# Kernel tuning notes

Hardware: AMD Instinct MI355X
Metric: run time of the kernel (lower is better)

Reference implementation:

```python
import jax, jax.numpy as jnp
import numpy as np

ALPHA = 0.9
T = 809          # doc_len_limit hard-coded in fofe_tricontext_encoder
M = 16           # opt['max_len'] (cand_len_limit)
BN_EPS = 1e-5


def _cand_indices(T, M):
    # Enumeration order matches get_sample_index: outer over start s, inner over span.
    s_list, e_list = [], []
    for s in range(T):
        for span in range(min(M, T - s)):
            s_list.append(s)
            e_list.append(s + span)
    return np.asarray(s_list, np.int32), np.asarray(e_list, np.int32)

_S_IDX, _E_IDX = _cand_indices(T, M)          # [N_CANDS] = [12824]
_SPAN = (_E_IDX - _S_IDX).astype(np.int64)
# FOFE decay coefficient alpha^(e-s+1) for subtracting the prefix before the span
_COEF = (ALPHA ** (_SPAN + 1)).astype(np.float32)
# Lower-triangular FOFE prefix operator: A[t,k] = alpha^(t-k) for k<=t
_DIFF = np.subtract.outer(np.arange(T), np.arange(T))
_AFWD = np.where(_DIFF >= 0, ALPHA ** np.maximum(_DIFF, 0), 0.0).astype(np.float32)


def _bn(x, g, b, m, v):
    return (x - m) * jax.lax.rsqrt(v + BN_EPS) * g + b


def _forward(doc_emb, query_emb, W1, g1, b1, m1, v1, W2, g2, b2, m2, v2, W3):
    B, Tt, Dd = doc_emb.shape
    A = jnp.asarray(_AFWD)
    # forward FOFE prefixes F[t] = sum_{k<=t} alpha^(t-k) x[k]; inverse FOFE suffixes
    F = jnp.einsum('tk,bkd->btd', A, doc_emb)          # [B,T,Dd]
    R = jnp.einsum('tk,bkd->btd', A.T, doc_emb)        # [B,T,Dd]
    Fp = jnp.concatenate([jnp.zeros((B, 1, Dd), F.dtype), F], axis=1)   # Fp[:,s]=F[s-1]
    Rp = jnp.concatenate([R, jnp.zeros((B, 1, Dd), R.dtype)], axis=1)   # Rp[:,e+1]
    s_idx = jnp.asarray(_S_IDX)
    e_idx = jnp.asarray(_E_IDX)
    coef = jnp.asarray(_COEF)
    lctx = Fp[:, s_idx]                                 # left context excl cand
    cand = F[:, e_idx] - coef[None, :, None] * Fp[:, s_idx]  # FOFE of span [s,e]
    rctx = Rp[:, e_idx + 1]                             # right context excl cand
    doc_fofe = jnp.concatenate([lctx, cand, rctx], axis=-1)  # [B,N,3*Dd]
    # query FOFE (fofe_linear): z = sum_t alpha^(Lq-1-t) q[t]
    Lq = query_emb.shape[1]
    w = (ALPHA ** jnp.arange(Lq - 1, -1, -1, dtype=jnp.float32))
    qf = jnp.einsum('t,btd->bd', w, query_emb)          # [B,E]
    N = doc_fofe.shape[1]
    qf_b = jnp.broadcast_to(qf[:, None, :], (B, N, qf.shape[-1]))
    dq = jnp.concatenate([doc_fofe, qf_b], axis=-1)     # [B,N,3*Dd+E]
    x = dq.reshape(B * N, -1)
    h = jax.nn.relu(_bn(x @ W1.T, g1, b1, m1, v1))      # 1x1 conv == GEMM
    h = jax.nn.relu(_bn(h @ W2.T, g2, b2, m2, v2))
    out = (h @ W3.T).reshape(B, N, 2)                   # 2 class scores per candidate
    return out


def setup_inputs() -> dict:
    key = jax.random.key(0)
    ks = jax.random.split(key, 13)
    B, Lq, Dd, E = 4, 30, 304, 300
    Cin, H4, H2 = 3 * Dd + E, 1024, 512
    return {
        'doc_emb': jax.random.normal(ks[0], (B, T, Dd), jnp.float32),
        'query_emb': jax.random.normal(ks[1], (B, Lq, E), jnp.float32),
        'W1': jax.random.normal(ks[2], (H4, Cin), jnp.float32) / np.sqrt(Cin),
        'g1': jax.random.normal(ks[3], (H4,), jnp.float32),
        'b1': jax.random.normal(ks[4], (H4,), jnp.float32),
        'm1': jax.random.normal(ks[5], (H4,), jnp.float32),
        'v1': jax.random.uniform(ks[6], (H4,), jnp.float32),
        'W2': jax.random.normal(ks[7], (H2, H4), jnp.float32) / np.sqrt(H4),
        'g2': jax.random.normal(ks[8], (H2,), jnp.float32),
        'b2': jax.random.normal(ks[9], (H2,), jnp.float32),
        'm2': jax.random.normal(ks[10], (H2,), jnp.float32),
        'v2': jax.random.uniform(ks[11], (H2,), jnp.float32),
        'W3': jax.random.normal(ks[12], (2, H2), jnp.float32) / np.sqrt(H2),
    }


def reference(doc_emb, query_emb, W1, g1, b1, m1, v1, W2, g2, b2, m2, v2, W3):
    return _forward(doc_emb, query_emb, W1, g1, b1, m1, v1, W2, g2, b2, m2, v2, W3)
```

## Files before the change

kernel.cpp:

```cpp
#include <hip/hip_runtime.h>
#include <hip/hip_fp16.h>
#include <string.h>

#define T_LEN   809
#define DD      304
#define EE      300
#define LQ      30
#define NCAND   12824
#define NPAD    12928
#define CIN     1212
#define H1      1024
#define H2      512
#define BATCH   4
#define MROWS_F (BATCH * NPAD)
#define KS      320
#define TPAD    3328
#define NROWS_U 3240

#define MP_SCAN0   0
#define MP_W1      416
#define MP_W2      4256
#define MP_BIAS2   6304
#define MP_BASE    6306
#define MP_RMAP    7330
#define MP_TOTAL   7532

__device__ __constant__ float c_coef[16] = {
  0.9f, 0.81f, 0.729f, 0.6561f, 0.59049f, 0.531441f, 0.4782969f, 0.43046721f,
  0.387420489f, 0.3486784401f, 0.31381059609f, 0.282429536481f,
  0.2541865828329f, 0.22876792454961f, 0.205891132094649f, 0.1853020188851841f
};

__device__ __forceinline__ unsigned short f2h(float f) {
  const __half h = __float2half(f);
  return __half_as_ushort(h);
}
__device__ __forceinline__ unsigned int hadd2u(unsigned int a, unsigned int b) {
  const __half2 r = __hadd2(*reinterpret_cast<const __half2*>(&a),
                            *reinterpret_cast<const __half2*>(&b));
  return *reinterpret_cast<const unsigned int*>(&r);
}
__device__ __forceinline__ unsigned int comb2h(unsigned int ul, unsigned int uc,
                                               unsigned int ue, __half2 ncf2) {
  const __half2 t = __hfma2(*reinterpret_cast<const __half2*>(&uc), ncf2,
                            *reinterpret_cast<const __half2*>(&ue));
  const __half2 r = __hadd2(*reinterpret_cast<const __half2*>(&ul), t);
  unsigned int ru = *reinterpret_cast<const unsigned int*>(&r);
  ru &= ~(((ru >> 15) & 0x10001u) * 0xFFFFu);
  return ru;
}

typedef const __attribute__((address_space(1))) unsigned int GU32;
typedef __attribute__((address_space(3))) unsigned int LU32;
__device__ __forceinline__ void async16(const unsigned short* g, unsigned short* l) {
  __builtin_amdgcn_global_load_lds((GU32*)g, (LU32*)l, 16, 0, 0);
}

__global__ __launch_bounds__(256) void k_prep(const float* __restrict__ doc,
                                              const float* __restrict__ qe,
                                              const float* __restrict__ W1,
                                              const float* __restrict__ g1,
                                              const float* __restrict__ b1,
                                              const float* __restrict__ m1,
                                              const float* __restrict__ v1,
                                              const float* __restrict__ W2,
                                              const float* __restrict__ g2,
                                              const float* __restrict__ b2,
                                              const float* __restrict__ m2,
                                              const float* __restrict__ v2,
                                              unsigned short* __restrict__ Fz,
                                              unsigned short* __restrict__ Rz,
                                              unsigned short* __restrict__ Wlc,
                                              unsigned short* __restrict__ Wr,
                                              unsigned short* __restrict__ W2b,
                                              float* __restrict__ bias2,
                                              float* __restrict__ baseW,
                                              unsigned int* __restrict__ rowmap)
{
  __shared__ float qs[EE];
  const int vb  = blockIdx.x;
  const int tid = threadIdx.x;

  if (vb < MP_W1) {
    const int dchunk = vb & 1;
    const int rest   = vb >> 1;
    const int tchunk = rest % 26;
    const int b      = (rest / 26) & 3;
    const int dir    = rest / 104;
    const int d  = dchunk * 256 + tid;
    const int t0 = tchunk * 32;
    if (dir == 0) {
      if (tchunk == 0 && d < KS) Fz[((size_t)b * 810) * KS + d] = 0;
      if (d >= DD) return;
      const float* db = doc + (size_t)b * T_LEN * DD + d;
      int start = t0 - 96; if (start < 0) start = 0;
      int end = t0 + 31; if (end > T_LEN - 1) end = T_LEN - 1;
      float s = 0.f;
      for (int t = start; t <= end; ++t) {
        s = fmaf(0.9f, s, db[(size_t)t * DD]);
        if (t >= t0) Fz[((size_t)b * 810 + 1 + t) * KS + d] = f2h(s);
      }
    } else {
      if (tchunk == 0 && d < KS) Rz[((size_t)b * 810 + 809) * KS + d] = 0;
      if (d >= DD) return;
      const float* db = doc + (size_t)b * T_LEN * DD + d;
      int t1 = t0 + 31; if (t1 > T_LEN - 1) t1 = T_LEN - 1;
      int start = t1 + 96; if (start > T_LEN - 1) start = T_LEN - 1;
      float s = 0.f;
      for (int t = start; t >= t0; --t) {
        s = fmaf(0.9f, s, db[(size_t)t * DD]);
        if (t <= t1) Rz[((size_t)b * 810 + t) * KS + d] = f2h(s);
      }
    }
  } else if (vb < MP_W2) {
    const int e = (vb - MP_W1) * 256 + tid;
    const int j = e / KS;
    const int k = e - j * KS;
    int jj, koff; unsigned short* dst; size_t idx;
    if (j < 1024)      { jj = j;        koff = k;       dst = Wlc; idx = (size_t)j * KS + k; }
    else if (j < 2048) { jj = j - 1024; koff = 304 + k; dst = Wlc; idx = (size_t)j * KS + k; }
    else               { jj = j - 2048; koff = 608 + k; dst = Wr;  idx = (size_t)(j - 2048) * KS + k; }
    float w = 0.f;
    if (k < 304) w = W1[(size_t)jj * CIN + koff] * g1[jj] * rsqrtf(v1[jj] + 1e-5f);
    dst[idx] = f2h(w);
  } else if (vb < MP_BIAS2) {
    const int e = (vb - MP_W2) * 256 + tid;
    const int j = e >> 10;
    const int k = e & 1023;
    const float w = W2[(size_t)j * H1 + k] * g2[j] * rsqrtf(v2[j] + 1e-5f);
    W2b[(size_t)j * H1 + k] = f2h(w);
  } else if (vb < MP_BASE) {
    const int i = (vb - MP_BIAS2) * 256 + tid;
    if (i < H2) {
      const float s = g2[i] * rsqrtf(v2[i] + 1e-5f);
      bias2[i] = b2[i] - m2[i] * s;
    }
  } else if (vb < MP_RMAP) {
    const int flat = vb - MP_BASE;
    const int b  = flat >> 8;
    const int jg = flat & 255;
    const float* q = qe + (size_t)b * LQ * EE;
    for (int k = tid; k < EE; k += 256) {
      float s = 0.f;
      for (int t = 0; t < LQ; ++t) s = fmaf(s, 0.9f, q[(size_t)t * EE + k]);
      qs[k] = s;
    }
    __syncthreads();
    const int wv   = tid >> 6;
    const int lane = tid & 63;
    const int j = jg * 4 + wv;
    const float* w = W1 + (size_t)j * CIN + 912;
    float acc = 0.f;
    for (int k = lane; k < EE; k += 64) acc = fmaf(qs[k], w[k], acc);
    #pragma unroll
    for (int off = 32; off; off >>= 1) acc += __shfl_down(acc, off);
    if (lane == 0) {
      const float sc = g1[j] * rsqrtf(v1[j] + 1e-5f);
      baseW[(size_t)b * 2048 + j]        = b1[j] - m1[j] * sc + acc * sc;
      baseW[(size_t)b * 2048 + 1024 + j] = 0.f;
    }
  } else {
    const int g = (vb - MP_RMAP) * 256 + tid;
    const int b  = g / NPAD;
    const int rr = g - b * NPAD;
    unsigned int mv = 0;
    if (rr < NCAND) {
      int s, span;
      if (rr < 12704) { s = rr >> 4; span = rr & 15; }
      else {
        const int x = rr - 12704;
        int d = 0;
        while (d < 14 && x >= (15 * (d + 1) - ((d + 1) * d) / 2)) ++d;
        span = x - (15 * d - (d * (d - 1)) / 2);
        s = 794 + d;
      }
      const unsigned int srow = (unsigned int)(b * 810 + s);
      const unsigned int erow = (unsigned int)(b * 810 + s + span + 1);
      mv = srow | (erow << 12) | ((unsigned int)span << 24);
    }
    rowmap[g] = mv;
  }
}

typedef __attribute__((ext_vector_type(8))) short frag8;
typedef __attribute__((ext_vector_type(4))) float f32x4;

#define GEMM_KLOOP(A_, B_, K_)                                                   \
  __shared__ __align__(16) unsigned short As[128 * 32];                          \
  __shared__ __align__(16) unsigned short Bs[128 * 32];                          \
  const int tid  = threadIdx.x;                                                  \
  const int lane = tid & 63;                                                     \
  const int wv   = tid >> 6;                                                     \
  const int wm   = wv & 1, wn = wv >> 1;                                         \
  const int lr = lane >> 2;                                                      \
  const int lc = lane & 3;                                                       \
  const int sc = lc ^ ((lr >> 1) & 3);                                           \
  const unsigned short* gA = A_ + ((size_t)bm * 128 + wv * 32 + lr) * K_ + sc * 8; \
  const unsigned short* gB = B_ + ((size_t)bn * 128 + wv * 32 + lr) * K_ + sc * 8; \
  const size_t row16 = (size_t)16 * K_;                                          \
  unsigned short* lA0 = &As[wv * 1024];                                          \
  unsigned short* lB0 = &Bs[wv * 1024];                                          \
  f32x4 acc[4][4];                                                               \
  _Pragma("unroll")                                                              \
  for (int i = 0; i < 4; ++i)                                                    \
    _Pragma("unroll")                                                            \
    for (int j = 0; j < 4; ++j) acc[i][j] = (f32x4){0.f, 0.f, 0.f, 0.f};         \
  const int arow = lane & 15;                                                    \
  const int pg   = (lane >> 4) ^ ((arow >> 1) & 3);                              \
  const int aoff = (wm * 64 + arow) * 32 + pg * 8;                               \
  const int boff = (wn * 64 + arow) * 32 + pg * 8;                               \
  for (int kc = 0; kc < K_; kc += 32) {                                          \
    __syncthreads();                                                             \
    async16(gA + kc,         lA0);                                               \
    async16(gA + kc + row16, lA0 + 512);                                         \
    async16(gB + kc,         lB0);                                               \
    async16(gB + kc + row16, lB0 + 512);                                         \
    __syncthreads();                                                             \
    frag8 a[4], b[4];                                                            \
    _Pragma("unroll")                                                            \
    for (int i = 0; i < 4; ++i) a[i] = *(const frag8*)&As[aoff + i * 512];       \
    _Pragma("unroll")                                                            \
    for (int i = 0; i < 4; ++i) b[i] = *(const frag8*)&Bs[boff + i * 512];       \
    _Pragma("unroll")                                                            \
    for (int i = 0; i < 4; ++i)                                                  \
      _Pragma("unroll")                                                          \
      for (int j = 0; j < 4; ++j)                                                \
        acc[i][j] = __builtin_amdgcn_mfma_f32_16x16x32_f16(a[i], b[j], acc[i][j], 0, 0, 0); \
  }

__global__ __launch_bounds__(256, 4) void k_ugemm(const unsigned short* __restrict__ Fz,
                                                  const unsigned short* __restrict__ Wlc,
                                                  const unsigned short* __restrict__ Rz,
                                                  const unsigned short* __restrict__ Wr,
                                                  const float* __restrict__ baseW,
                                                  unsigned short* __restrict__ UF,
                                                  unsigned short* __restrict__ UR)
{
  int bx = blockIdx.x;
  const int isUF = (bx < 416);
  const unsigned short *Ap, *Bp; unsigned short* Cp; int bn, bm, Nout;
  if (isUF) { Ap = Fz; Bp = Wlc; Cp = UF; bn = bx & 15; bm = bx >> 4; Nout = 2048; }
  else { bx -= 416; Ap = Rz; Bp = Wr; Cp = UR; bn = bx & 7; bm = bx >> 3; Nout = 1024; }
  GEMM_KLOOP(Ap, Bp, KS)
  const int crow0 = bm * 128 + wm * 64 + ((lane >> 4) << 2);
  const int ccol0 = bn * 128 + wn * 64 + arow;
  #pragma unroll
  for (int i = 0; i < 4; ++i)
    #pragma unroll
    for (int j = 0; j < 4; ++j) {
      const int col = ccol0 + j * 16;
      #pragma unroll
      for (int r = 0; r < 4; ++r) {
        const int row = crow0 + i * 16 + r;
        float v = acc[i][j][r];
        if (isUF) {
          int bb = row / 810; if (bb > 3) bb = 3;
          v += baseW[(size_t)bb * 2048 + col];
        }
        Cp[(size_t)row * Nout + col] = f2h(v);
      }
    }
}

__global__ __launch_bounds__(256) void k_ucr(const unsigned short* __restrict__ UF,
                                             const unsigned short* __restrict__ UR,
                                             unsigned short* __restrict__ UCR)
{
  const int c = blockIdx.x * 256 + threadIdx.x;
  if (c >= NROWS_U * 128) return;
  const int t  = c >> 7;
  const int kk = (c & 127) * 8;
  const uint4 a = *(const uint4*)(UF + (size_t)t * 2048 + 1024 + kk);
  const uint4 b = *(const uint4*)(UR + (size_t)t * 1024 + kk);
  uint4 o;
  o.x = hadd2u(a.x, b.x);
  o.y = hadd2u(a.y, b.y);
  o.z = hadd2u(a.z, b.z);
  o.w = hadd2u(a.w, b.w);
  *(uint4*)(UCR + (size_t)t * 1024 + kk) = o;
}

__global__ __launch_bounds__(512, 4) void k_gemm2f(const unsigned short* __restrict__ UF,
                                                   const unsigned short* __restrict__ UCR,
                                                   const unsigned short* __restrict__ W2b,
                                                   const unsigned int* __restrict__ rowmap,
                                                   const float* __restrict__ bias,
                                                   const float* __restrict__ W3,
                                                   float* __restrict__ P)
{
  __shared__ __align__(16) unsigned short As[2 * 128 * 32];
  __shared__ __align__(16) unsigned short Bs[2 * 256 * 32];

  const int orig = blockIdx.x;
  const int wg = (orig & 7) * 101 + (orig >> 3);
  const int bm = wg >> 1, bn = wg & 1;

  const int tid  = threadIdx.x;
  const int lane = tid & 63;
  const int w    = tid >> 6;
  const int wm   = w & 1;
  const int wn   = w >> 1;
  const int arow = lane & 15;
  const int lr   = lane >> 2;
  const int lc   = lane & 3;
  const int sc   = lc ^ ((lr >> 1) & 3);

  const int rA    = tid >> 2;
  const int cA    = tid & 3;
  const int physA = cA ^ ((rA >> 1) & 3);
  const unsigned int mv = rowmap[bm * 128 + rA];
  const __half2 ncf2 = __float2half2_rn(-c_coef[mv >> 24]);
  const unsigned short* pUL = UF  + (size_t)(mv & 4095) * 2048 + cA * 8;
  const unsigned short* pUE = UCR + (size_t)((mv >> 12) & 4095) * 1024 + cA * 8;

  const unsigned short* gB = W2b + ((size_t)(bn * 256 + w * 32 + lr)) * H1 + sc * 8;

  const int pg   = (lane >> 4) ^ ((arow >> 1) & 3);
  const int aoff = (wm * 64 + arow) * 32 + pg * 8;
  const int boff = (wn * 64 + arow) * 32 + pg * 8;

  f32x4 acc[4][4];
  #pragma unroll
  for (int i = 0; i < 4; ++i)
    #pragma unroll
    for (int j = 0; j < 4; ++j) acc[i][j] = (f32x4){0.f, 0.f, 0.f, 0.f};

  uint4 vulN = *(const uint4*)(pUL);
  uint4 vucN = *(const uint4*)(pUL + 1024);
  uint4 vueN = *(const uint4*)(pUE);
  {
    unsigned short* lB = &Bs[w * 1024];
    async16(gB,           lB);
    async16(gB + 16 * H1, lB + 512);
  }
  {
    uint4 o;
    o.x = comb2h(vulN.x, vucN.x, vueN.x, ncf2);
    o.y = comb2h(vulN.y, vucN.y, vueN.y, ncf2);
    o.z = comb2h(vulN.z, vucN.z, vueN.z, ncf2);
    o.w = comb2h(vulN.w, vucN.w, vueN.w, ncf2);
    *(uint4*)&As[rA * 32 + physA * 8] = o;
  }
  vulN = *(const uint4*)(pUL + 32);
  vucN = *(const uint4*)(pUL + 1024 + 32);
  vueN = *(const uint4*)(pUE + 32);
  asm volatile("s_waitcnt vmcnt(3) lgkmcnt(0)" ::: "memory");
  __builtin_amdgcn_sched_barrier(0);

  for (int k = 0; k < 32; ++k) {
    const int cur = k & 1, nxt = cur ^ 1;
    __builtin_amdgcn_s_barrier();
    __builtin_amdgcn_sched_barrier(0);
    if (k < 31) {
      const int kn = (k + 1) * 32;
      unsigned short* lB = &Bs[nxt * 8192 + w * 1024];
      async16(gB + kn,           lB);
      async16(gB + kn + 16 * H1, lB + 512);
      __builtin_amdgcn_sched_barrier(0);
      asm volatile("s_waitcnt vmcnt(2)" ::: "memory");
      __builtin_amdgcn_sched_barrier(0);
      uint4 o;
      o.x = comb2h(vulN.x, vucN.x, vueN.x, ncf2);
      o.y = comb2h(vulN.y, vucN.y, vueN.y, ncf2);
      o.z = comb2h(vulN.z, vucN.z, vueN.z, ncf2);
      o.w = comb2h(vulN.w, vucN.w, vueN.w, ncf2);
      *(uint4*)&As[nxt * 4096 + rA * 32 + physA * 8] = o;
      if (k < 30) {
        const int kg = (k + 2) * 32;
        vulN = *(const uint4*)(pUL + kg);
        vucN = *(const uint4*)(pUL + 1024 + kg);
        vueN = *(const uint4*)(pUE + kg);
      }
    }
    __builtin_amdgcn_sched_barrier(0);
    frag8 a[4], b[4];
    #pragma unroll
    for (int i = 0; i < 4; ++i) a[i] = *(const frag8*)&As[cur * 4096 + aoff + i * 512];
    #pragma unroll
    for (int j = 0; j < 4; ++j) b[j] = *(const frag8*)&Bs[cur * 8192 + boff + j * 512];
    __builtin_amdgcn_s_setprio(1);
    #pragma unroll
    for (int i = 0; i < 4; ++i)
      #pragma unroll
      for (int j = 0; j < 4; ++j)
        acc[i][j] = __builtin_amdgcn_mfma_f32_16x16x32_f16(a[i], b[j], acc[i][j], 0, 0, 0);
    __builtin_amdgcn_s_setprio(0);
    __builtin_amdgcn_sched_barrier(0);
    if (k < 30)       { asm volatile("s_waitcnt vmcnt(3)" ::: "memory"); }
    else if (k == 30) { asm volatile("s_waitcnt vmcnt(0)" ::: "memory"); }
    __builtin_amdgcn_sched_barrier(0);
  }

  __syncthreads();
  float* redf = (float*)As;

  float bj[4], w0v[4], w1v[4];
  #pragma unroll
  for (int j = 0; j < 4; ++j) {
    const int col = bn * 256 + wn * 64 + j * 16 + arow;
    bj[j]  = bias[col];
    w0v[j] = W3[col];
    w1v[j] = W3[H2 + col];
  }
  const int grp = lane >> 4;
  #pragma unroll
  for (int i = 0; i < 4; ++i)
    #pragma unroll
    for (int r = 0; r < 4; ++r) {
      float q0 = 0.f, q1 = 0.f;
      #pragma unroll
      for (int j = 0; j < 4; ++j) {
        float v = acc[i][j][r] + bj[j];
        v = v > 0.f ? v : 0.f;
        q0 = fmaf(v, w0v[j], q0);
        q1 = fmaf(v, w1v[j], q1);
      }
      #pragma unroll
      for (int m = 1; m < 16; m <<= 1) { q0 += __shfl_xor(q0, m); q1 += __shfl_xor(q1, m); }
      if (arow == 0) {
        const int rl = wm * 64 + i * 16 + grp * 4 + r;
        redf[(rl * 4 + wn) * 2]     = q0;
        redf[(rl * 4 + wn) * 2 + 1] = q1;
      }
    }
  __syncthreads();
  if (tid < 256) {
    const int rl = tid >> 1, s = tid & 1;
    const float v = redf[(rl * 4 + 0) * 2 + s] + redf[(rl * 4 + 1) * 2 + s]
                  + redf[(rl * 4 + 2) * 2 + s] + redf[(rl * 4 + 3) * 2 + s];
    P[((size_t)(bm * 128 + rl)) * 4 + bn * 2 + s] = v;
  }
}

__global__ __launch_bounds__(256) void k_fin(const float* __restrict__ P, float* __restrict__ out)
{
  const int row = blockIdx.x * 256 + threadIdx.x;
  if (row >= MROWS_F) return;
  const int b = row / NPAD;
  const int rr = row - b * NPAD;
  if (rr >= NCAND) return;
  const float4 pa = ((const float4*)P)[row];
  float* o = out + ((size_t)b * NCAND + rr) * 2;
  o[0] = pa.x + pa.z;
  o[1] = pa.y + pa.w;
}

extern "C" void kernel_launch(void* const* d_in, const int* in_sizes, int n_in,
                              void* d_out, int out_size, void* d_ws, size_t ws_size,
                              hipStream_t stream)
{
  const float* doc = (const float*)d_in[0];
  const float* qe  = (const float*)d_in[1];
  const float* W1  = (const float*)d_in[2];
  const float* g1  = (const float*)d_in[3];
  const float* b1  = (const float*)d_in[4];
  const float* m1  = (const float*)d_in[5];
  const float* v1  = (const float*)d_in[6];
  const float* W2  = (const float*)d_in[7];
  const float* g2  = (const float*)d_in[8];
  const float* b2  = (const float*)d_in[9];
  const float* m2  = (const float*)d_in[10];
  const float* v2  = (const float*)d_in[11];
  const float* W3  = (const float*)d_in[12];
  float* out = (float*)d_out;

  char* ws = (char*)d_ws;
  size_t off = 0;
  auto alloc = [&](size_t bytes) -> void* {
    void* p = ws + off;
    off = (off + bytes + 255) & ~(size_t)255;
    return p;
  };
  unsigned short* Fz    = (unsigned short*)alloc((size_t)TPAD * KS * 2);
  unsigned short* Rz    = (unsigned short*)alloc((size_t)TPAD * KS * 2);
  unsigned short* Wlc   = (unsigned short*)alloc((size_t)2048 * KS * 2);
  unsigned short* Wr    = (unsigned short*)alloc((size_t)1024 * KS * 2);
  unsigned short* W2b   = (unsigned short*)alloc((size_t)H2 * H1 * 2);
  float*          bias2 = (float*)alloc((size_t)H2 * 4);
  float*          baseW = (float*)alloc((size_t)BATCH * 2048 * 4);
  unsigned short* UF    = (unsigned short*)alloc((size_t)TPAD * 2048 * 2);
  unsigned short* UR    = (unsigned short*)alloc((size_t)TPAD * 1024 * 2);
  unsigned short* UCR   = (unsigned short*)alloc((size_t)NROWS_U * 1024 * 2);
  unsigned int*   rowmap= (unsigned int*)alloc((size_t)MROWS_F * 4);
  float*          P     = (float*)alloc((size_t)MROWS_F * 4 * 4);
  (void)ws_size;

  k_prep<<<dim3(MP_TOTAL), 256, 0, stream>>>(doc, qe, W1, g1, b1, m1, v1,
                                             W2, g2, b2, m2, v2,
                                             Fz, Rz, Wlc, Wr, W2b, bias2, baseW, rowmap);
  k_ugemm<<<dim3(416 + 208), 256, 0, stream>>>(Fz, Wlc, Rz, Wr, baseW, UF, UR);
  k_ucr<<<dim3((NROWS_U * 128 + 255) / 256), 256, 0, stream>>>(UF, UR, UCR);
  k_gemm2f<<<dim3(808), 512, 0, stream>>>(UF, UCR, W2b, rowmap, bias2, W3, P);
  k_fin<<<dim3((MROWS_F + 255) / 256), 256, 0, stream>>>(P, out);
}
```

Baseline: 214.9 us.

## Double-buffer LDS in the U GEMM k-loop and split FOFE scan warmup loop

Turns the shared GEMM_KLOOP macro used by the U-projection GEMM into a double-buffered pipeline. The next K-tile's async global-to-LDS copies are issued before the MFMAs on the current tile, and each iteration uses one barrier instead of two. It also splits the FOFE prefix and suffix scans into a warmup loop with no stores and a store loop without the per-step branch, both unrolled. The double buffer doubles LDS per block in that kernel, which could cut occupancy under launch_bounds(256,4). The renames in the MLP kernel are cosmetic.

```diff
diff --git a/kernel.cpp b/kernel.cpp
--- a/kernel.cpp
+++ b/kernel.cpp
@@ -96,9 +96,13 @@
       int start = t0 - 96; if (start < 0) start = 0;
       int end = t0 + 31; if (end > T_LEN - 1) end = T_LEN - 1;
       float s = 0.f;
-      for (int t = start; t <= end; ++t) {
+      int t = start;
+      #pragma unroll 4
+      for (; t < t0; ++t) s = fmaf(0.9f, s, db[(size_t)t * DD]);
+      #pragma unroll 4
+      for (; t <= end; ++t) {
         s = fmaf(0.9f, s, db[(size_t)t * DD]);
-        if (t >= t0) Fz[((size_t)b * 810 + 1 + t) * KS + d] = f2h(s);
+        Fz[((size_t)b * 810 + 1 + t) * KS + d] = f2h(s);
       }
     } else {
       if (tchunk == 0 && d < KS) Rz[((size_t)b * 810 + 809) * KS + d] = 0;
@@ -107,9 +111,13 @@
       int t1 = t0 + 31; if (t1 > T_LEN - 1) t1 = T_LEN - 1;
       int start = t1 + 96; if (start > T_LEN - 1) start = T_LEN - 1;
       float s = 0.f;
-      for (int t = start; t >= t0; --t) {
+      int t = start;
+      #pragma unroll 4
+      for (; t > t1; --t) s = fmaf(0.9f, s, db[(size_t)t * DD]);
+      #pragma unroll 4
+      for (; t >= t0; --t) {
         s = fmaf(0.9f, s, db[(size_t)t * DD]);
-        if (t <= t1) Rz[((size_t)b * 810 + t) * KS + d] = f2h(s);
+        Rz[((size_t)b * 810 + t) * KS + d] = f2h(s);
       }
     }
   } else if (vb < MP_W2) {
@@ -186,8 +194,8 @@
 typedef __attribute__((ext_vector_type(4))) float f32x4;
 
 #define GEMM_KLOOP(A_, B_, K_)                                                   \
-  __shared__ __align__(16) unsigned short As[128 * 32];                          \
-  __shared__ __align__(16) unsigned short Bs[128 * 32];                          \
+  __shared__ __align__(16) unsigned short As[2 * 128 * 32];                      \
+  __shared__ __align__(16) unsigned short Bs[2 * 128 * 32];                      \
   const int tid  = threadIdx.x;                                                  \
   const int lane = tid & 63;                                                     \
   const int wv   = tid >> 6;                                                     \
@@ -198,8 +206,6 @@
   const unsigned short* gA = A_ + ((size_t)bm * 128 + wv * 32 + lr) * K_ + sc * 8; \
   const unsigned short* gB = B_ + ((size_t)bn * 128 + wv * 32 + lr) * K_ + sc * 8; \
   const size_t row16 = (size_t)16 * K_;                                          \
-  unsigned short* lA0 = &As[wv * 1024];                                          \
-  unsigned short* lB0 = &Bs[wv * 1024];                                          \
   f32x4 acc[4][4];                                                               \
   _Pragma("unroll")                                                              \
   for (int i = 0; i < 4; ++i)                                                    \
@@ -209,23 +215,38 @@
   const int pg   = (lane >> 4) ^ ((arow >> 1) & 3);                              \
   const int aoff = (wm * 64 + arow) * 32 + pg * 8;                               \
   const int boff = (wn * 64 + arow) * 32 + pg * 8;                               \
+  async16(gA,         &As[wv * 1024]);                                           \
+  async16(gA + row16, &As[wv * 1024 + 512]);                                     \
+  async16(gB,         &Bs[wv * 1024]);                                           \
+  async16(gB + row16, &Bs[wv * 1024 + 512]);                                     \
+  asm volatile("s_waitcnt vmcnt(0)" ::: "memory");                               \
+  __builtin_amdgcn_sched_barrier(0);                                             \
   for (int kc = 0; kc < K_; kc += 32) {                                          \
-    __syncthreads();                                                             \
-    async16(gA + kc,         lA0);                                               \
-    async16(gA + kc + row16, lA0 + 512);                                         \
-    async16(gB + kc,         lB0);                                               \
-    async16(gB + kc + row16, lB0 + 512);                                         \
-    __syncthreads();                                                             \
+    const int cb = (kc >> 5) & 1, nb = cb ^ 1;                                   \
+    __builtin_amdgcn_s_barrier();                                                \
+    __builtin_amdgcn_sched_barrier(0);                                           \
+    if (kc + 32 < K_) {                                                          \
+      async16(gA + kc + 32,         &As[nb * 4096 + wv * 1024]);                 \
+      async16(gA + kc + 32 + row16, &As[nb * 4096 + wv * 1024 + 512]);           \
+      async16(gB + kc + 32,         &Bs[nb * 4096 + wv * 1024]);                 \
+      async16(gB + kc + 32 + row16, &Bs[nb * 4096 + wv * 1024 + 512]);           \
+    }                                                                            \
+    __builtin_amdgcn_sched_barrier(0);                                           \
     frag8 a[4], b[4];                                                            \
     _Pragma("unroll")                                                            \
-    for (int i = 0; i < 4; ++i) a[i] = *(const frag8*)&As[aoff + i * 512];       \
+    for (int i = 0; i < 4; ++i) a[i] = *(const frag8*)&As[cb * 4096 + aoff + i * 512]; \
     _Pragma("unroll")                                                            \
-    for (int i = 0; i < 4; ++i) b[i] = *(const frag8*)&Bs[boff + i * 512];       \
+    for (int i = 0; i < 4; ++i) b[i] = *(const frag8*)&Bs[cb * 4096 + boff + i * 512]; \
+    __builtin_amdgcn_s_setprio(1);                                               \
     _Pragma("unroll")                                                            \
     for (int i = 0; i < 4; ++i)                                                  \
       _Pragma("unroll")                                                          \
       for (int j = 0; j < 4; ++j)                                                \
         acc[i][j] = __builtin_amdgcn_mfma_f32_16x16x32_f16(a[i], b[j], acc[i][j], 0, 0, 0); \
+    __builtin_amdgcn_s_setprio(0);                                               \
+    __builtin_amdgcn_sched_barrier(0);                                           \
+    if (kc + 32 < K_) { asm volatile("s_waitcnt vmcnt(0)" ::: "memory"); }       \
+    __builtin_amdgcn_sched_barrier(0);                                           \
   }
 
 __global__ __launch_bounds__(256, 4) void k_ugemm(const unsigned short* __restrict__ Fz,
@@ -288,8 +309,8 @@
                                                    const float* __restrict__ W3,
                                                    float* __restrict__ P)
 {
-  __shared__ __align__(16) unsigned short As[2 * 128 * 32];
-  __shared__ __align__(16) unsigned short Bs[2 * 256 * 32];
+  __shared__ __align__(16) unsigned short As2[2 * 128 * 32];
+  __shared__ __align__(16) unsigned short Bs2[2 * 256 * 32];
 
   const int orig = blockIdx.x;
   const int wg = (orig & 7) * 101 + (orig >> 3);
@@ -329,7 +350,7 @@
   uint4 vucN = *(const uint4*)(pUL + 1024);
   uint4 vueN = *(const uint4*)(pUE);
   {
-    unsigned short* lB = &Bs[w * 1024];
+    unsigned short* lB = &Bs2[w * 1024];
     async16(gB,           lB);
     async16(gB + 16 * H1, lB + 512);
   }
@@ -339,7 +360,7 @@
     o.y = comb2h(vulN.y, vucN.y, vueN.y, ncf2);
     o.z = comb2h(vulN.z, vucN.z, vueN.z, ncf2);
     o.w = comb2h(vulN.w, vucN.w, vueN.w, ncf2);
-    *(uint4*)&As[rA * 32 + physA * 8] = o;
+    *(uint4*)&As2[rA * 32 + physA * 8] = o;
   }
   vulN = *(const uint4*)(pUL + 32);
   vucN = *(const uint4*)(pUL + 1024 + 32);
@@ -353,7 +374,7 @@
     __builtin_amdgcn_sched_barrier(0);
     if (k < 31) {
       const int kn = (k + 1) * 32;
-      unsigned short* lB = &Bs[nxt * 8192 + w * 1024];
+      unsigned short* lB = &Bs2[nxt * 8192 + w * 1024];
       async16(gB + kn,           lB);
       async16(gB + kn + 16 * H1, lB + 512);
       __builtin_amdgcn_sched_barrier(0);
@@ -364,7 +385,7 @@
       o.y = comb2h(vulN.y, vucN.y, vueN.y, ncf2);
       o.z = comb2h(vulN.z, vucN.z, vueN.z, ncf2);
       o.w = comb2h(vulN.w, vucN.w, vueN.w, ncf2);
-      *(uint4*)&As[nxt * 4096 + rA * 32 + physA * 8] = o;
+      *(uint4*)&As2[nxt * 4096 + rA * 32 + physA * 8] = o;
       if (k < 30) {
         const int kg = (k + 2) * 32;
         vulN = *(const uint4*)(pUL + kg);
@@ -375,9 +396,9 @@
     __builtin_amdgcn_sched_barrier(0);
     frag8 a[4], b[4];
     #pragma unroll
-    for (int i = 0; i < 4; ++i) a[i] = *(const frag8*)&As[cur * 4096 + aoff + i * 512];
-    #pragma unroll
-    for (int j = 0; j < 4; ++j) b[j] = *(const frag8*)&Bs[cur * 8192 + boff + j * 512];
+    for (int i = 0; i < 4; ++i) a[i] = *(const frag8*)&As2[cur * 4096 + aoff + i * 512];
+    #pragma unroll
+    for (int j = 0; j < 4; ++j) b[j] = *(const frag8*)&Bs2[cur * 8192 + boff + j * 512];
     __builtin_amdgcn_s_setprio(1);
     #pragma unroll
     for (int i = 0; i < 4; ++i)
@@ -392,7 +413,7 @@
   }
 
   __syncthreads();
-  float* redf = (float*)As;
+  float* redf = (float*)As2;
 
   float bj[4], w0v[4], w1v[4];
   #pragma unroll
```

After: 197.2 us. -8.3%, faster.
